# Performance work log

Hardware: AMD Instinct MI355X
Metric: run time of the kernel (lower is better)

The kernel has to match this reference:

```python
import jax, jax.numpy as jnp
import numpy as np

B, S, DM, H = 2, 4096, 512, 8
DEPTH = DM // H


def setup_inputs() -> dict:
    key = jax.random.key(0)
    ks = jax.random.split(key, 12)
    scale = 1.0 / np.sqrt(DM)
    return {
        "q": jax.random.normal(ks[0], (B, S, DM), jnp.float32),
        "k": jax.random.normal(ks[1], (B, S, DM), jnp.float32),
        "v": jax.random.normal(ks[2], (B, S, DM), jnp.float32),
        # padding-style mask: 1.0 = masked position, 0.0 = attend
        "mask": jax.random.bernoulli(ks[3], 0.1, (B, 1, 1, S)).astype(jnp.float32),
        "Wq": jax.random.normal(ks[4], (DM, DM), jnp.float32) * scale,
        "bq": jnp.zeros((DM,), jnp.float32),
        "Wk": jax.random.normal(ks[5], (DM, DM), jnp.float32) * scale,
        "bk": jnp.zeros((DM,), jnp.float32),
        "Wv": jax.random.normal(ks[6], (DM, DM), jnp.float32) * scale,
        "bv": jnp.zeros((DM,), jnp.float32),
        "Wo": jax.random.normal(ks[7], (DM, DM), jnp.float32) * scale,
        "bo": jnp.zeros((DM,), jnp.float32),
    }


def _split_heads(x):
    # [B, S, DM] -> [B, H, S, DEPTH]
    b, s, _ = x.shape
    return x.reshape(b, s, H, DEPTH).transpose(0, 2, 1, 3)


def reference(q, k, v, mask, Wq, bq, Wk, bk, Wv, bv, Wo, bo):
    qh = _split_heads(q @ Wq + bq)   # [B,H,S,D]
    kh = _split_heads(k @ Wk + bk)
    vh = _split_heads(v @ Wv + bv)
    logits = jnp.einsum("bhqd,bhkd->bhqk", qh, kh) / jnp.sqrt(
        jnp.asarray(DEPTH, qh.dtype))
    logits = logits + mask * (-1e9)
    attn = jax.nn.softmax(logits, axis=-1)          # [B,H,Sq,Sk]
    out = jnp.einsum("bhqk,bhkd->bhqd", attn, vh)   # [B,H,S,D]
    out = out.transpose(0, 2, 1, 3).reshape(q.shape[0], -1, DM)
    return out @ Wo + bo
```

## Files before the change

### kernel.cpp

```cpp
#include <hip/hip_runtime.h>
#include <math.h>

#define BDIM 2
#define SDIM 4096
#define DMODEL 512
#define NHEAD 8
#define DHEAD 64
#define MROWS (BDIM * SDIM)

typedef __attribute__((ext_vector_type(8))) short short8;
typedef __attribute__((ext_vector_type(4))) float f32x4;
typedef __attribute__((ext_vector_type(16))) float f32x16;
typedef __attribute__((ext_vector_type(4))) int i32x4;

#define MFMA16(a, b, c) __builtin_amdgcn_mfma_f32_16x16x32_bf16((a), (b), (c), 0, 0, 0)
#define MFMA32(a, b, c) __builtin_amdgcn_mfma_f32_32x32x16_bf16((a), (b), (c), 0, 0, 0)
#define EXP2F(x) __builtin_amdgcn_exp2f(x)

#define SCALE2 0.18033688011112042f
#define MASKMUL -1.442695040e9f
#define M0C 16.0f

__device__ inline void bf16_split(float x, short& h, short& l) {
  unsigned u = __float_as_uint(x);
  h = (short)(u >> 16);
  float hf = __uint_as_float(u & 0xffff0000u);
  l = (short)(__float_as_uint(x - hf) >> 16);
}

__global__ __launch_bounds__(256) void wsplit_kernel(
    const float* __restrict__ W0, const float* __restrict__ W1,
    const float* __restrict__ W2, const float* __restrict__ W3,
    short* __restrict__ T0h, short* __restrict__ T0l, short* __restrict__ T1h,
    short* __restrict__ T1l, short* __restrict__ T2h, short* __restrict__ T2l,
    short* __restrict__ T3h, short* __restrict__ T3l) {
  __shared__ short Th[64 * 72], Tl[64 * 72];
  const int tid = threadIdx.x;
  const int k0 = blockIdx.x * 64;
  const int n0 = blockIdx.y * 64;
  const int z = blockIdx.z;
  const float* W = (z == 0) ? W0 : (z == 1) ? W1 : (z == 2) ? W2 : W3;
  short* Oh = (z == 0) ? T0h : (z == 1) ? T1h : (z == 2) ? T2h : T3h;
  short* Ol = (z == 0) ? T0l : (z == 1) ? T1l : (z == 2) ? T2l : T3l;

  {
    const int r = tid >> 2;
    const int c16 = (tid & 3) * 16;
    short8 h0, h1, l0, l1;
#pragma unroll
    for (int g = 0; g < 2; g++) {
      const f32x4 a = *(const f32x4*)(W + (size_t)(k0 + r) * DMODEL + n0 + c16 + g * 8);
      const f32x4 b = *(const f32x4*)(W + (size_t)(k0 + r) * DMODEL + n0 + c16 + g * 8 + 4);
      short8& hh = g ? h1 : h0;
      short8& ll = g ? l1 : l0;
#pragma unroll
      for (int j = 0; j < 4; j++) {
        short x, y;
        bf16_split(a[j], x, y);
        hh[j] = x;
        ll[j] = y;
        bf16_split(b[j], x, y);
        hh[4 + j] = x;
        ll[4 + j] = y;
      }
    }
    *(short8*)&Th[r * 72 + c16] = h0;
    *(short8*)&Th[r * 72 + c16 + 8] = h1;
    *(short8*)&Tl[r * 72 + c16] = l0;
    *(short8*)&Tl[r * 72 + c16 + 8] = l1;
  }
  __syncthreads();
  {
    const int n = tid >> 2;
    const int kc = (tid & 3) * 16;
    short8 h0, h1, l0, l1;
#pragma unroll
    for (int i = 0; i < 8; i++) {
      h0[i] = Th[(kc + i) * 72 + n];
      h1[i] = Th[(kc + 8 + i) * 72 + n];
      l0[i] = Tl[(kc + i) * 72 + n];
      l1[i] = Tl[(kc + 8 + i) * 72 + n];
    }
    short* dh = Oh + (size_t)(n0 + n) * DMODEL + k0 + kc;
    short* dl = Ol + (size_t)(n0 + n) * DMODEL + k0 + kc;
    *(short8*)dh = h0;
    *(short8*)(dh + 8) = h1;
    *(short8*)dl = l0;
    *(short8*)(dl + 8) = l1;
  }
}

template <int MODE>
__global__ __launch_bounds__(256, 4) void proj_mfma_kernel(
    const float* __restrict__ X, const short* __restrict__ Wth,
    const short* __restrict__ Wtl, const float* __restrict__ bias,
    float* __restrict__ out, short* __restrict__ oh, short* __restrict__ ol) {
  __shared__ short Xh[64 * 72], Xl[64 * 72];
  __shared__ short Wh[64 * 72], Wl[64 * 72];

  const int tid = threadIdx.x;
  const int lane = tid & 63;
  const int w = tid >> 6;
  const int lane15 = lane & 15;
  const int quad = lane >> 4;
  const int wm = (w >> 1) * 32;
  const int wn = (w & 1) * 32;
  const int m0 = blockIdx.x * 64;
  const int n0 = blockIdx.y * 64;

  f32x4 c[2][2];
#pragma unroll
  for (int mt = 0; mt < 2; mt++)
#pragma unroll
    for (int nt = 0; nt < 2; nt++) c[mt][nt] = (f32x4){0.f, 0.f, 0.f, 0.f};

  const int sr = tid >> 2;
  const int sc16 = (tid & 3) * 16;

  for (int k0 = 0; k0 < DMODEL; k0 += 64) {
    {
      short8 h0, h1, l0, l1;
#pragma unroll
      for (int g = 0; g < 2; g++) {
        const f32x4 a =
            *(const f32x4*)(X + (size_t)(m0 + sr) * DMODEL + k0 + sc16 + g * 8);
        const f32x4 b = *(const f32x4*)(X + (size_t)(m0 + sr) * DMODEL + k0 +
                                        sc16 + g * 8 + 4);
        short8& hh = g ? h1 : h0;
        short8& ll = g ? l1 : l0;
#pragma unroll
        for (int j = 0; j < 4; j++) {
          short x, y;
          bf16_split(a[j], x, y);
          hh[j] = x;
          ll[j] = y;
          bf16_split(b[j], x, y);
          hh[4 + j] = x;
          ll[4 + j] = y;
        }
      }
      *(short8*)&Xh[sr * 72 + sc16] = h0;
      *(short8*)&Xh[sr * 72 + sc16 + 8] = h1;
      *(short8*)&Xl[sr * 72 + sc16] = l0;
      *(short8*)&Xl[sr * 72 + sc16 + 8] = l1;

      const short* wsh = Wth + (size_t)(n0 + sr) * DMODEL + k0 + sc16;
      const short* wsl = Wtl + (size_t)(n0 + sr) * DMODEL + k0 + sc16;
      *(short8*)&Wh[sr * 72 + sc16] = *(const short8*)wsh;
      *(short8*)&Wh[sr * 72 + sc16 + 8] = *(const short8*)(wsh + 8);
      *(short8*)&Wl[sr * 72 + sc16] = *(const short8*)wsl;
      *(short8*)&Wl[sr * 72 + sc16 + 8] = *(const short8*)(wsl + 8);
    }
    __syncthreads();

#pragma unroll
    for (int ks = 0; ks < 2; ks++) {
      short8 ah[2], al[2], bh[2], bl[2];
#pragma unroll
      for (int mt = 0; mt < 2; mt++) {
        const int xo = (wm + mt * 16 + lane15) * 72 + ks * 32 + quad * 8;
        ah[mt] = *(const short8*)&Xh[xo];
        al[mt] = *(const short8*)&Xl[xo];
      }
#pragma unroll
      for (int nt = 0; nt < 2; nt++) {
        const int wo = (wn + nt * 16 + lane15) * 72 + ks * 32 + quad * 8;
        bh[nt] = *(const short8*)&Wh[wo];
        bl[nt] = *(const short8*)&Wl[wo];
      }
#pragma unroll
      for (int mt = 0; mt < 2; mt++)
#pragma unroll
        for (int nt = 0; nt < 2; nt++) {
          c[mt][nt] = MFMA16(ah[mt], bh[nt], c[mt][nt]);
          c[mt][nt] = MFMA16(ah[mt], bl[nt], c[mt][nt]);
          c[mt][nt] = MFMA16(al[mt], bh[nt], c[mt][nt]);
        }
    }
    __syncthreads();
  }

#pragma unroll
  for (int nt = 0; nt < 2; nt++) {
    const int n = n0 + wn + nt * 16 + lane15;
    const float bb = bias[n];
#pragma unroll
    for (int mt = 0; mt < 2; mt++)
#pragma unroll
      for (int r = 0; r < 4; r++) {
        const int m = m0 + wm + mt * 16 + quad * 4 + r;
        const float val = c[mt][nt][r] + bb;
        if (MODE == 1) {
          const int bidx = m >> 12;
          const int s = m & 4095;
          const int hh = n >> 6;
          const int d = n & 63;
          const size_t off =
              ((size_t)(bidx * NHEAD + hh) * SDIM + s) * DHEAD + d;
          short x, y;
          bf16_split(val, x, y);
          oh[off] = x;
          ol[off] = y;
        } else {
          out[(size_t)m * DMODEL + n] = val;
        }
      }
  }
}

__global__ __launch_bounds__(256) void vtrans_kernel(
    const short* __restrict__ vh, const short* __restrict__ vl,
    short* __restrict__ vth, short* __restrict__ vtl) {
  __shared__ short Th[64 * 72], Tl[64 * 72];
  const int tid = threadIdx.x;
  const int s0 = blockIdx.x * 64;
  const int h = blockIdx.y;
  const int b = blockIdx.z;
  const size_t base = (size_t)(b * NHEAD + h) * SDIM * DHEAD;

  {
    const int s = tid >> 2;
    const int c = tid & 3;
    const short* srcH = vh + base + (size_t)(s0 + s) * DHEAD + c * 16;
    const short* srcL = vl + base + (size_t)(s0 + s) * DHEAD + c * 16;
    *(short8*)&Th[s * 72 + c * 16] = *(const short8*)srcH;
    *(short8*)&Th[s * 72 + c * 16 + 8] = *(const short8*)(srcH + 8);
    *(short8*)&Tl[s * 72 + c * 16] = *(const short8*)srcL;
    *(short8*)&Tl[s * 72 + c * 16 + 8] = *(const short8*)(srcL + 8);
  }
  __syncthreads();
  {
    const int d = tid & 63;
    const int cw = tid >> 6;
    short8 a0, a1, b0, b1;
#pragma unroll
    for (int i = 0; i < 8; i++) {
      a0[i] = Th[(cw * 16 + i) * 72 + d];
      a1[i] = Th[(cw * 16 + 8 + i) * 72 + d];
      b0[i] = Tl[(cw * 16 + i) * 72 + d];
      b1[i] = Tl[(cw * 16 + 8 + i) * 72 + d];
    }
    short* dstH = vth + base + (size_t)d * SDIM + s0 + cw * 16;
    short* dstL = vtl + base + (size_t)d * SDIM + s0 + cw * 16;
    *(short8*)dstH = a0;
    *(short8*)(dstH + 8) = a1;
    *(short8*)dstL = b0;
    *(short8*)(dstL + 8) = b1;
  }
}

#define KP 72
#define VP 72
#define PP 68

__global__ __launch_bounds__(256, 2) void flash_attn_kernel(
    const short* __restrict__ qhh, const short* __restrict__ qhl,
    const short* __restrict__ khh, const short* __restrict__ khl,
    const short* __restrict__ vth, const short* __restrict__ vtl,
    const float* __restrict__ mask, float* __restrict__ ctx) {
  __shared__ short Ksh[64 * KP], Ksl[64 * KP];
  __shared__ short Vsh[64 * VP], Vsl[64 * VP];
  __shared__ int Ps[128 * PP];

  const int tid = threadIdx.x;
  const int lane = tid & 63;
  const int w = tid >> 6;
  const int l31 = lane & 31;
  const int half = lane >> 5;
  const int q0 = blockIdx.x * 128;
  const int h = blockIdx.y;
  const int b = blockIdx.z;

  const size_t base = (size_t)(b * NHEAD + h) * SDIM * DHEAD;
  const short* Qh = qhh + base;
  const short* Ql = qhl + base;
  const short* Kh = khh + base;
  const short* Kl = khl + base;
  const short* Vh = vth + base;
  const short* Vl = vtl + base;
  const float* mb = mask + (size_t)b * SDIM;

  short8 qfh[4], qfl[4];
  {
    const size_t row = q0 + w * 32 + l31;
#pragma unroll
    for (int c = 0; c < 4; c++) {
      qfh[c] = *(const short8*)(Qh + row * DHEAD + c * 16 + half * 8);
      qfl[c] = *(const short8*)(Ql + row * DHEAD + c * 16 + half * 8);
    }
  }

  f32x16 o[2], lsum;
#pragma unroll
  for (int i = 0; i < 16; i++) {
    o[0][i] = 0.f;
    o[1][i] = 0.f;
    lsum[i] = 0.f;
  }

  short8 onesb;
#pragma unroll
  for (int j = 0; j < 8; j++) onesb[j] = (short)0x3F80;

  const int sr = tid >> 2;
  const int sc = (tid & 3) * 16;

  for (int kt = 0; kt < SDIM / 64; kt++) {
    const int k0 = kt * 64;
    {
      const short8 a0 = *(const short8*)(Kh + (size_t)(k0 + sr) * DHEAD + sc);
      const short8 a1 = *(const short8*)(Kh + (size_t)(k0 + sr) * DHEAD + sc + 8);
      const short8 b0 = *(const short8*)(Kl + (size_t)(k0 + sr) * DHEAD + sc);
      const short8 b1 = *(const short8*)(Kl + (size_t)(k0 + sr) * DHEAD + sc + 8);
      const short8 c0 = *(const short8*)(Vh + (size_t)sr * SDIM + k0 + sc);
      const short8 c1 = *(const short8*)(Vh + (size_t)sr * SDIM + k0 + sc + 8);
      const short8 d0 = *(const short8*)(Vl + (size_t)sr * SDIM + k0 + sc);
      const short8 d1 = *(const short8*)(Vl + (size_t)sr * SDIM + k0 + sc + 8);
      *(short8*)&Ksh[sr * KP + sc] = a0;
      *(short8*)&Ksh[sr * KP + sc + 8] = a1;
      *(short8*)&Ksl[sr * KP + sc] = b0;
      *(short8*)&Ksl[sr * KP + sc + 8] = b1;
      *(short8*)&Vsh[sr * VP + sc] = c0;
      *(short8*)&Vsh[sr * VP + sc + 8] = c1;
      *(short8*)&Vsl[sr * VP + sc] = d0;
      *(short8*)&Vsl[sr * VP + sc + 8] = d1;
    }
    float mv[2];
#pragma unroll
    for (int t = 0; t < 2; t++)
      mv[t] = fmaf(mb[k0 + t * 32 + l31], MASKMUL, -M0C);
    __syncthreads();

#pragma unroll
    for (int t = 0; t < 2; t++) {
      f32x16 acc;
#pragma unroll
      for (int i = 0; i < 16; i++) acc[i] = 0.f;
#pragma unroll
      for (int c = 0; c < 4; c++) {
        const int koff = (t * 32 + l31) * KP + c * 16 + half * 8;
        const short8 kbh = *(const short8*)&Ksh[koff];
        const short8 kbl = *(const short8*)&Ksl[koff];
        acc = MFMA32(qfh[c], kbh, acc);
        acc = MFMA32(qfh[c], kbl, acc);
        acc = MFMA32(qfl[c], kbh, acc);
      }
#pragma unroll
      for (int reg = 0; reg < 16; reg++) {
        const int row = (reg & 3) + 8 * (reg >> 2) + 4 * half;
        const float p = EXP2F(fmaf(acc[reg], SCALE2, mv[t]));
        short ph, pl;
        bf16_split(p, ph, pl);
        Ps[(w * 32 + row) * PP + t * 32 + l31] =
            (((int)(unsigned short)ph) << 16) | (int)(unsigned short)pl;
      }
    }

    short8 pah[4], pal[4];
#pragma unroll
    for (int kc = 0; kc < 4; kc++) {
      const int* pr = &Ps[(w * 32 + l31) * PP + kc * 16 + half * 8];
      const i32x4 w0 = *(const i32x4*)pr;
      const i32x4 w1 = *(const i32x4*)(pr + 4);
      short8 ph, pl;
#pragma unroll
      for (int j = 0; j < 4; j++) {
        ph[j] = (short)((unsigned)w0[j] >> 16);
        pl[j] = (short)(w0[j] & 0xffff);
        ph[4 + j] = (short)((unsigned)w1[j] >> 16);
        pl[4 + j] = (short)(w1[j] & 0xffff);
      }
      pah[kc] = ph;
      pal[kc] = pl;
    }

#pragma unroll
    for (int kc = 0; kc < 4; kc++) {
      lsum = MFMA32(pah[kc], onesb, lsum);
      lsum = MFMA32(pal[kc], onesb, lsum);
    }

#pragma unroll
    for (int t2 = 0; t2 < 2; t2++)
#pragma unroll
      for (int kc = 0; kc < 4; kc++) {
        const int voff = (t2 * 32 + l31) * VP + kc * 16 + half * 8;
        const short8 vbh = *(const short8*)&Vsh[voff];
        const short8 vbl = *(const short8*)&Vsl[voff];
        o[t2] = MFMA32(pah[kc], vbh, o[t2]);
        o[t2] = MFMA32(pah[kc], vbl, o[t2]);
        o[t2] = MFMA32(pal[kc], vbh, o[t2]);
      }
    __syncthreads();
  }

  float inv[16];
#pragma unroll
  for (int reg = 0; reg < 16; reg++) inv[reg] = 1.f / lsum[reg];
#pragma unroll
  for (int t2 = 0; t2 < 2; t2++)
#pragma unroll
    for (int reg = 0; reg < 16; reg++) {
      const int q = q0 + w * 32 + (reg & 3) + 8 * (reg >> 2) + 4 * half;
      const int d = t2 * 32 + l31;
      ctx[((size_t)b * SDIM + q) * DMODEL + h * DHEAD + d] =
          o[t2][reg] * inv[reg];
    }
}

extern "C" void kernel_launch(void* const* d_in, const int* in_sizes, int n_in,
                              void* d_out, int out_size, void* d_ws,
                              size_t ws_size, hipStream_t stream) {
  const float* q = (const float*)d_in[0];
  const float* k = (const float*)d_in[1];
  const float* v = (const float*)d_in[2];
  const float* mask = (const float*)d_in[3];
  const float* Wq = (const float*)d_in[4];
  const float* bq = (const float*)d_in[5];
  const float* Wk = (const float*)d_in[6];
  const float* bk = (const float*)d_in[7];
  const float* Wv = (const float*)d_in[8];
  const float* bv = (const float*)d_in[9];
  const float* Wo = (const float*)d_in[10];
  const float* bo = (const float*)d_in[11];
  float* out = (float*)d_out;

  char* W = (char*)d_ws;
  const size_t SZB = (size_t)MROWS * DMODEL * sizeof(short);
  short* q_h = (short*)(W + 0 * SZB);
  short* q_l = (short*)(W + 1 * SZB);
  short* k_h = (short*)(W + 2 * SZB);
  short* k_l = (short*)(W + 3 * SZB);
  short* v_h = (short*)(W + 4 * SZB);
  short* v_l = (short*)(W + 5 * SZB);
  short* vt_h = (short*)(W + 6 * SZB);
  short* vt_l = (short*)(W + 7 * SZB);
  float* ctx = (float*)(W + 4 * SZB);

  const size_t WSZ = (size_t)DMODEL * DMODEL * sizeof(short);
  char* WT = W + 8 * SZB;
  short* wtq_h = (short*)(WT + 0 * WSZ);
  short* wtq_l = (short*)(WT + 1 * WSZ);
  short* wtk_h = (short*)(WT + 2 * WSZ);
  short* wtk_l = (short*)(WT + 3 * WSZ);
  short* wtv_h = (short*)(WT + 4 * WSZ);
  short* wtv_l = (short*)(WT + 5 * WSZ);
  short* wto_h = (short*)(WT + 6 * WSZ);
  short* wto_l = (short*)(WT + 7 * WSZ);

  wsplit_kernel<<<dim3(DMODEL / 64, DMODEL / 64, 4), 256, 0, stream>>>(
      Wq, Wk, Wv, Wo, wtq_h, wtq_l, wtk_h, wtk_l, wtv_h, wtv_l, wto_h, wto_l);

  const dim3 gproj(MROWS / 64, DMODEL / 64);
  proj_mfma_kernel<1><<<gproj, 256, 0, stream>>>(q, wtq_h, wtq_l, bq, nullptr,
                                                 q_h, q_l);
  proj_mfma_kernel<1><<<gproj, 256, 0, stream>>>(k, wtk_h, wtk_l, bk, nullptr,
                                                 k_h, k_l);
  proj_mfma_kernel<1><<<gproj, 256, 0, stream>>>(v, wtv_h, wtv_l, bv, nullptr,
                                                 v_h, v_l);

  vtrans_kernel<<<dim3(SDIM / 64, NHEAD, BDIM), 256, 0, stream>>>(v_h, v_l,
                                                                  vt_h, vt_l);

  flash_attn_kernel<<<dim3(SDIM / 128, NHEAD, BDIM), 256, 0, stream>>>(
      q_h, q_l, k_h, k_l, vt_h, vt_l, mask, ctx);

  proj_mfma_kernel<0><<<gproj, 256, 0, stream>>>(ctx, wto_h, wto_l, bo, out,
                                                 nullptr, nullptr);
}
```

Measured before the change: 407.5 us.

## Transpose attention MFMAs to keep probabilities in registers, drop LDS P staging

The QK^T and PV MFMAs swap operand order so each lane holds one query column of S^T. The exponentiated probabilities can then be rearranged with a cross-half lane shuffle and fed directly as the B operand, instead of round-tripping through a shared-memory P buffer. Row sums are accumulated in scalar registers, replacing the ones-vector MFMAs, and the mask is staged in a small shared array. Launch bounds rise to 4 blocks per CU now that LDS use shrinks, which adds register pressure and shuffle overhead in exchange.

```diff
diff --git a/kernel.cpp b/kernel.cpp
--- a/kernel.cpp
+++ b/kernel.cpp
@@ -11,7 +11,6 @@
 typedef __attribute__((ext_vector_type(8))) short short8;
 typedef __attribute__((ext_vector_type(4))) float f32x4;
 typedef __attribute__((ext_vector_type(16))) float f32x16;
-typedef __attribute__((ext_vector_type(4))) int i32x4;
 
 #define MFMA16(a, b, c) __builtin_amdgcn_mfma_f32_16x16x32_bf16((a), (b), (c), 0, 0, 0)
 #define MFMA32(a, b, c) __builtin_amdgcn_mfma_f32_32x32x16_bf16((a), (b), (c), 0, 0, 0)
@@ -251,16 +250,15 @@
 
 #define KP 72
 #define VP 72
-#define PP 68
-
-__global__ __launch_bounds__(256, 2) void flash_attn_kernel(
+
+__global__ __launch_bounds__(256, 4) void flash_attn_kernel(
     const short* __restrict__ qhh, const short* __restrict__ qhl,
     const short* __restrict__ khh, const short* __restrict__ khl,
     const short* __restrict__ vth, const short* __restrict__ vtl,
     const float* __restrict__ mask, float* __restrict__ ctx) {
   __shared__ short Ksh[64 * KP], Ksl[64 * KP];
   __shared__ short Vsh[64 * VP], Vsl[64 * VP];
-  __shared__ int Ps[128 * PP];
+  __shared__ float Ms[64];
 
   const int tid = threadIdx.x;
   const int lane = tid & 63;
@@ -290,17 +288,13 @@
     }
   }
 
-  f32x16 o[2], lsum;
+  f32x16 o[2];
 #pragma unroll
   for (int i = 0; i < 16; i++) {
     o[0][i] = 0.f;
     o[1][i] = 0.f;
-    lsum[i] = 0.f;
-  }
-
-  short8 onesb;
-#pragma unroll
-  for (int j = 0; j < 8; j++) onesb[j] = (short)0x3F80;
+  }
+  float lacc = 0.f;
 
   const int sr = tid >> 2;
   const int sc = (tid & 3) * 16;
@@ -325,10 +319,7 @@
       *(short8*)&Vsl[sr * VP + sc] = d0;
       *(short8*)&Vsl[sr * VP + sc + 8] = d1;
     }
-    float mv[2];
-#pragma unroll
-    for (int t = 0; t < 2; t++)
-      mv[t] = fmaf(mb[k0 + t * 32 + l31], MASKMUL, -M0C);
+    if (tid < 64) Ms[tid] = fmaf(mb[k0 + tid], MASKMUL, -M0C);
     __syncthreads();
 
 #pragma unroll
@@ -341,70 +332,72 @@
         const int koff = (t * 32 + l31) * KP + c * 16 + half * 8;
         const short8 kbh = *(const short8*)&Ksh[koff];
         const short8 kbl = *(const short8*)&Ksl[koff];
-        acc = MFMA32(qfh[c], kbh, acc);
-        acc = MFMA32(qfh[c], kbl, acc);
-        acc = MFMA32(qfl[c], kbh, acc);
-      }
-#pragma unroll
-      for (int reg = 0; reg < 16; reg++) {
-        const int row = (reg & 3) + 8 * (reg >> 2) + 4 * half;
-        const float p = EXP2F(fmaf(acc[reg], SCALE2, mv[t]));
-        short ph, pl;
-        bf16_split(p, ph, pl);
-        Ps[(w * 32 + row) * PP + t * 32 + l31] =
-            (((int)(unsigned short)ph) << 16) | (int)(unsigned short)pl;
-      }
-    }
-
-    short8 pah[4], pal[4];
-#pragma unroll
-    for (int kc = 0; kc < 4; kc++) {
-      const int* pr = &Ps[(w * 32 + l31) * PP + kc * 16 + half * 8];
-      const i32x4 w0 = *(const i32x4*)pr;
-      const i32x4 w1 = *(const i32x4*)(pr + 4);
-      short8 ph, pl;
-#pragma unroll
-      for (int j = 0; j < 4; j++) {
-        ph[j] = (short)((unsigned)w0[j] >> 16);
-        pl[j] = (short)(w0[j] & 0xffff);
-        ph[4 + j] = (short)((unsigned)w1[j] >> 16);
-        pl[4 + j] = (short)(w1[j] & 0xffff);
-      }
-      pah[kc] = ph;
-      pal[kc] = pl;
-    }
-
-#pragma unroll
-    for (int kc = 0; kc < 4; kc++) {
-      lsum = MFMA32(pah[kc], onesb, lsum);
-      lsum = MFMA32(pal[kc], onesb, lsum);
-    }
-
-#pragma unroll
-    for (int t2 = 0; t2 < 2; t2++)
-#pragma unroll
-      for (int kc = 0; kc < 4; kc++) {
-        const int voff = (t2 * 32 + l31) * VP + kc * 16 + half * 8;
-        const short8 vbh = *(const short8*)&Vsh[voff];
-        const short8 vbl = *(const short8*)&Vsl[voff];
-        o[t2] = MFMA32(pah[kc], vbh, o[t2]);
-        o[t2] = MFMA32(pah[kc], vbl, o[t2]);
-        o[t2] = MFMA32(pal[kc], vbh, o[t2]);
-      }
+        acc = MFMA32(kbh, qfh[c], acc);
+        acc = MFMA32(kbh, qfl[c], acc);
+        acc = MFMA32(kbl, qfh[c], acc);
+      }
+
+      float pt[16];
+      float tsum = 0.f;
+#pragma unroll
+      for (int g = 0; g < 4; g++) {
+        const f32x4 mq = *(const f32x4*)&Ms[t * 32 + g * 8 + half * 4];
+#pragma unroll
+        for (int i = 0; i < 4; i++) {
+          const float p = EXP2F(fmaf(acc[g * 4 + i], SCALE2, mq[i]));
+          pt[g * 4 + i] = p;
+          tsum += p;
+        }
+      }
+      lacc += tsum;
+
+#pragma unroll
+      for (int kc2 = 0; kc2 < 2; kc2++) {
+        const int bse = kc2 * 8;
+        float sendv[4], recvv[4];
+#pragma unroll
+        for (int i = 0; i < 4; i++)
+          sendv[i] = half ? pt[bse + i] : pt[bse + 4 + i];
+#pragma unroll
+        for (int i = 0; i < 4; i++) recvv[i] = __shfl_xor(sendv[i], 32, 64);
+        float bl[8];
+#pragma unroll
+        for (int i = 0; i < 4; i++) {
+          bl[i] = half ? recvv[i] : pt[bse + i];
+          bl[4 + i] = half ? pt[bse + 4 + i] : recvv[i];
+        }
+        short8 ph, pl;
+#pragma unroll
+        for (int j = 0; j < 8; j++) {
+          short x, y;
+          bf16_split(bl[j], x, y);
+          ph[j] = x;
+          pl[j] = y;
+        }
+        const int KC = t * 32 + kc2 * 16;
+#pragma unroll
+        for (int t2 = 0; t2 < 2; t2++) {
+          const int voff = (t2 * 32 + l31) * VP + KC + half * 8;
+          const short8 vbh = *(const short8*)&Vsh[voff];
+          const short8 vbl = *(const short8*)&Vsl[voff];
+          o[t2] = MFMA32(vbh, ph, o[t2]);
+          o[t2] = MFMA32(vbh, pl, o[t2]);
+          o[t2] = MFMA32(vbl, ph, o[t2]);
+        }
+      }
+    }
     __syncthreads();
   }
 
-  float inv[16];
-#pragma unroll
-  for (int reg = 0; reg < 16; reg++) inv[reg] = 1.f / lsum[reg];
+  const float ltot = lacc + __shfl_xor(lacc, 32, 64);
+  const float inv = 1.f / ltot;
+  const int q = q0 + w * 32 + l31;
 #pragma unroll
   for (int t2 = 0; t2 < 2; t2++)
 #pragma unroll
     for (int reg = 0; reg < 16; reg++) {
-      const int q = q0 + w * 32 + (reg & 3) + 8 * (reg >> 2) + 4 * half;
-      const int d = t2 * 32 + l31;
-      ctx[((size_t)b * SDIM + q) * DMODEL + h * DHEAD + d] =
-          o[t2][reg] * inv[reg];
+      const int d = t2 * 32 + (reg & 3) + 8 * (reg >> 2) + 4 * half;
+      ctx[((size_t)b * SDIM + q) * DMODEL + h * DHEAD + d] = o[t2][reg] * inv;
     }
 }
 
```

Result: slower. 526.8 us (+29.3%).
